# Optimization experiments

Hardware: AMD Instinct MI355X
Metric: run time of the kernel (lower is better)

The kernel has to match this reference:

```python
import jax, jax.numpy as jnp
import numpy as np


def setup_inputs() -> dict:
    key = jax.random.key(0)
    k1, k2 = jax.random.split(key)
    B, S, D, T = 64, 512, 768, 384
    hidden_states = jax.random.normal(k1, (B, S, D), dtype=jnp.float32)
    # sorted per-row segment ids: each subtoken belongs to a token index in [0, T)
    segment_ids = jnp.sort(jax.random.randint(k2, (B, S), 0, T), axis=-1)
    return {"hidden_states": hidden_states, "segment_ids": segment_ids, "num_tokens": T}


def reference(hidden_states, segment_ids, num_tokens):
    # Segment-mean of subtoken embeddings into token embeddings.
    # Equivalent to the original running-mean loop:
    #   prev + (next - prev) / n_subtoken_per_token  == mean over the group.
    B, S, D = hidden_states.shape
    # flatten batch into segment ids so one segment_sum handles all sequences
    flat_ids = (segment_ids + jnp.arange(B, dtype=segment_ids.dtype)[:, None] * num_tokens).reshape(-1)
    sums = jax.ops.segment_sum(hidden_states.reshape(-1, D), flat_ids,
                               num_segments=B * num_tokens)  # [B*T, D]
    counts = jax.ops.segment_sum(jnp.ones((B * S,), dtype=hidden_states.dtype), flat_ids,
                                 num_segments=B * num_tokens)  # [B*T]
    # tokens with no subtokens stay zero (original initializes with zeros)
    means = sums / jnp.maximum(counts, 1.0)[:, None]
    return means.reshape(B, num_tokens, D)
```

## Files before the change

### kernel.cpp

```cpp
#include <hip/hip_runtime.h>


#define TPW 4
#define WPB 4
#define TPB (TPW * WPB)

__global__ void table_kernel(const int* __restrict__ seg,
                             const int* __restrict__ num_tokens_p,
                             int* __restrict__ table,
                             int BS_total,
                             int BT) {
  const int T = num_tokens_p[0];
  const int B = BT / T;
  const int S = BS_total / B;
  int s = blockIdx.x * blockDim.x + threadIdx.x;
  if (s >= BS_total) return;
  const int b = s / S;
  const int cur = b * T + seg[s];
  const int prev = (s == 0) ? -1 : ((s - 1) / S) * T + seg[s - 1];
  for (int g = prev + 1; g <= cur; ++g) table[g] = s;
  if (s == BS_total - 1) {
    for (int g = cur + 1; g <= BT; ++g) table[g] = BS_total;
  }
}

template <int NCH>
__global__ __launch_bounds__(WPB * 64) void seg_mean_kernel(
    const float* __restrict__ hs,
    const int* __restrict__ table,
    float* __restrict__ out,
    int BT,
    int D4) {
  const int lane = threadIdx.x & 63;
  const int wid = threadIdx.x >> 6;
  const int g0 = (blockIdx.x * WPB + wid) * TPW;
  if (g0 >= BT) return;
  const int n = min(TPW, BT - g0);

  int bnd[TPW + 1];
#pragma unroll
  for (int i = 0; i <= TPW; ++i) bnd[i] = (i <= n) ? table[g0 + i] : 0;

  const float4* __restrict__ hs4 = (const float4*)hs;
  float4* __restrict__ out4 = (float4*)out;

  int r = bnd[0];
  for (int tok = 0; tok < n; ++tok) {
    const int rend = bnd[tok + 1];
    float4 acc[NCH];
#pragma unroll
    for (int c = 0; c < NCH; ++c) acc[c] = make_float4(0.f, 0.f, 0.f, 0.f);
    for (; r < rend; ++r) {
      const float4* __restrict__ p = hs4 + (size_t)r * D4 + lane;
#pragma unroll
      for (int c = 0; c < NCH; ++c) {
        float4 v = p[c * 64];
        acc[c].x += v.x; acc[c].y += v.y; acc[c].z += v.z; acc[c].w += v.w;
      }
    }
    const int cnt = rend - bnd[tok];
    const float inv = (cnt > 0) ? (1.0f / (float)cnt) : 0.0f;
    float4* __restrict__ q = out4 + (size_t)(g0 + tok) * D4 + lane;
#pragma unroll
    for (int c = 0; c < NCH; ++c) {
      q[c * 64] = make_float4(acc[c].x * inv, acc[c].y * inv,
                              acc[c].z * inv, acc[c].w * inv);
    }
  }
}

__global__ void seg_mean_fallback(const float* __restrict__ hs,
                                  const int* __restrict__ table,
                                  float* __restrict__ out,
                                  int D) {
  const int g = blockIdx.x;
  const int lo = table[g];
  const int hi = table[g + 1];
  const int cnt = hi - lo;
  const float inv = (cnt > 0) ? (1.0f / (float)cnt) : 0.0f;
  for (int d = threadIdx.x; d < D; d += blockDim.x) {
    float a = 0.f;
    for (int r = lo; r < hi; ++r) a += hs[(size_t)r * D + d];
    out[(size_t)g * D + d] = a * inv;
  }
}

extern "C" void kernel_launch(void* const* d_in, const int* in_sizes, int n_in,
                              void* d_out, int out_size, void* d_ws, size_t ws_size,
                              hipStream_t stream) {
  const float* hs = (const float*)d_in[0];
  const int* seg = (const int*)d_in[1];
  const int* num_tokens_p = (const int*)d_in[2];
  float* out = (float*)d_out;

  const int BS_total = in_sizes[1];
  const int D = in_sizes[0] / in_sizes[1];
  const int BT = out_size / D;

  int* table = (int*)d_ws;

  const int threads1 = 256;
  const int grid1 = (BS_total + threads1 - 1) / threads1;
  hipLaunchKernelGGL(table_kernel, dim3(grid1), dim3(threads1), 0, stream,
                     seg, num_tokens_p, table, BS_total, BT);

  const int D4 = D / 4;
  const int grid2 = (BT + TPB - 1) / TPB;
  if (D % 4 == 0 && D4 % 64 == 0 && D4 / 64 >= 1 && D4 / 64 <= 4) {
    switch (D4 / 64) {
      case 1:
        hipLaunchKernelGGL(seg_mean_kernel<1>, dim3(grid2), dim3(WPB * 64), 0,
                           stream, hs, table, out, BT, D4);
        break;
      case 2:
        hipLaunchKernelGGL(seg_mean_kernel<2>, dim3(grid2), dim3(WPB * 64), 0,
                           stream, hs, table, out, BT, D4);
        break;
      case 3:
        hipLaunchKernelGGL(seg_mean_kernel<3>, dim3(grid2), dim3(WPB * 64), 0,
                           stream, hs, table, out, BT, D4);
        break;
      default:
        hipLaunchKernelGGL(seg_mean_kernel<4>, dim3(grid2), dim3(WPB * 64), 0,
                           stream, hs, table, out, BT, D4);
        break;
    }
  } else {
    hipLaunchKernelGGL(seg_mean_fallback, dim3(BT), dim3(256), 0, stream,
                       hs, table, out, D);
  }
}
```

Baseline: 179.9 us.

## Batch row loads across token boundaries and use nontemporal output stores

The per-token accumulation loop becomes a single walk over the wave's whole row range. Up to four rows are loaded at once before they are accumulated, and each token is flushed when its boundary is crossed. This raises memory-level parallelism, since the old loop issued one row's loads at a time and stalled at every token boundary. Output stores are now nontemporal so they do not pollute the cache. The flush logic is more complex and runs inside the unrolled loop, which may increase register pressure and code size.

```diff
diff --git a/kernel.cpp b/kernel.cpp
--- a/kernel.cpp
+++ b/kernel.cpp
@@ -1,9 +1,12 @@
 #include <hip/hip_runtime.h>
 
+
+typedef float v4f __attribute__((ext_vector_type(4)));
 
 #define TPW 4
 #define WPB 4
 #define TPB (TPW * WPB)
+#define RCHUNK 4
 
 __global__ void table_kernel(const int* __restrict__ seg,
                              const int* __restrict__ num_tokens_p,
@@ -35,38 +38,76 @@
   const int wid = threadIdx.x >> 6;
   const int g0 = (blockIdx.x * WPB + wid) * TPW;
   if (g0 >= BT) return;
-  const int n = min(TPW, BT - g0);
+  const int ntok = min(TPW, BT - g0);
 
   int bnd[TPW + 1];
 #pragma unroll
-  for (int i = 0; i <= TPW; ++i) bnd[i] = (i <= n) ? table[g0 + i] : 0;
+  for (int i = 0; i <= TPW; ++i)
+    bnd[i] = table[g0 + ((i <= ntok) ? i : ntok)];
 
-  const float4* __restrict__ hs4 = (const float4*)hs;
-  float4* __restrict__ out4 = (float4*)out;
+  const v4f* __restrict__ hs4 = (const v4f*)hs;
+  v4f* __restrict__ out4 = (v4f*)out;
 
   int r = bnd[0];
-  for (int tok = 0; tok < n; ++tok) {
-    const int rend = bnd[tok + 1];
-    float4 acc[NCH];
+  const int rend = bnd[TPW];
+  int tok = 0;
+
+  v4f acc[NCH];
 #pragma unroll
-    for (int c = 0; c < NCH; ++c) acc[c] = make_float4(0.f, 0.f, 0.f, 0.f);
-    for (; r < rend; ++r) {
-      const float4* __restrict__ p = hs4 + (size_t)r * D4 + lane;
+  for (int c = 0; c < NCH; ++c) acc[c] = (v4f)(0.f);
+
+#define FLUSH_AT(R)                                                          \
+  while (tok < TPW && bnd[tok + 1] <= (R)) {                                 \
+    const int cnt = bnd[tok + 1] - bnd[tok];                                 \
+    const float inv = (cnt > 0) ? (1.0f / (float)cnt) : 0.0f;                \
+    if (tok < ntok) {                                                        \
+      v4f* __restrict__ q = out4 + (size_t)(g0 + tok) * D4 + lane;           \
+      _Pragma("unroll")                                                      \
+      for (int c = 0; c < NCH; ++c) {                                        \
+        v4f o = acc[c] * inv;                                                \
+        __builtin_nontemporal_store(o, q + c * 64);                          \
+      }                                                                      \
+    }                                                                        \
+    _Pragma("unroll")                                                        \
+    for (int c = 0; c < NCH; ++c) acc[c] = (v4f)(0.f);                       \
+    ++tok;                                                                   \
+  }
+
+  FLUSH_AT(r);
+
+  while (r < rend) {
+    const int m = min(RCHUNK, rend - r);
+    v4f v[RCHUNK][NCH];
 #pragma unroll
-      for (int c = 0; c < NCH; ++c) {
-        float4 v = p[c * 64];
-        acc[c].x += v.x; acc[c].y += v.y; acc[c].z += v.z; acc[c].w += v.w;
+    for (int j = 0; j < RCHUNK; ++j) {
+      if (j < m) {
+        const v4f* __restrict__ p = hs4 + (size_t)(r + j) * D4 + lane;
+#pragma unroll
+        for (int c = 0; c < NCH; ++c) v[j][c] = p[c * 64];
       }
     }
-    const int cnt = rend - bnd[tok];
-    const float inv = (cnt > 0) ? (1.0f / (float)cnt) : 0.0f;
-    float4* __restrict__ q = out4 + (size_t)(g0 + tok) * D4 + lane;
 #pragma unroll
-    for (int c = 0; c < NCH; ++c) {
-      q[c * 64] = make_float4(acc[c].x * inv, acc[c].y * inv,
-                              acc[c].z * inv, acc[c].w * inv);
+    for (int j = 0; j < RCHUNK; ++j) {
+      if (j < m) {
+#pragma unroll
+        for (int c = 0; c < NCH; ++c) acc[c] += v[j][c];
+        FLUSH_AT(r + j + 1);
+      }
     }
+    r += m;
   }
+
+  FLUSH_AT(rend);
+  while (tok < TPW) {
+    if (tok < ntok) {
+      v4f* __restrict__ q = out4 + (size_t)(g0 + tok) * D4 + lane;
+      const v4f z = (v4f)(0.f);
+#pragma unroll
+      for (int c = 0; c < NCH; ++c) __builtin_nontemporal_store(z, q + c * 64);
+    }
+    ++tok;
+  }
+#undef FLUSH_AT
 }
 
 __global__ void seg_mean_fallback(const float* __restrict__ hs,
```

New measurement: 182.7 us. Within noise of the previous version (+1.6%).
